# Kernel tuning notes

Hardware: AMD Instinct MI355X
Metric: run time of the kernel (lower is better)

The kernel has to match this reference:

```python
import jax, jax.numpy as jnp
import numpy as np

NUM_LAYERS = 4
EPS = 1e-8


def setup_inputs() -> dict:
    key = jax.random.key(0)
    ks = jax.random.split(key, 7)
    N, D, H = 8192, 1024, 4096
    return {
        "x": jax.random.normal(ks[0], (N, D), jnp.float32),
        "fc1_W": jax.random.normal(ks[1], (H, D), jnp.float32) * 0.02,
        "fc1_b": jax.random.normal(ks[2], (H,), jnp.float32) * 0.02,
        "fc2_W": jax.random.normal(ks[3], (D, H), jnp.float32) * 0.02,
        "fc2_b": jax.random.normal(ks[4], (D,), jnp.float32) * 0.02,
        "comp_W": jax.random.normal(ks[5], (NUM_LAYERS + 1, D, D), jnp.float32) * 0.03,
        "comp_b": jax.random.normal(ks[6], (NUM_LAYERS + 1, D), jnp.float32) * 0.03,
    }


def _block(x, fc1_W, fc1_b, fc2_W, fc2_b):
    # fc2(dropout(fc1(x))) in eval mode; relu is defined but never applied
    h = x @ fc1_W.T + fc1_b
    return h @ fc2_W.T + fc2_b


def _compute_loss(z, W, b):
    # out = Linear(z); per-row cosine_similarity(out_i.unsqueeze(1), out_i.unsqueeze(0))
    # reduces broadcast dim 1 -> vector c[j] = out[j]*sum(out) / max(|out[j]|*sqrt(y)*||out||, eps)
    # which torch broadcasts into constant rows of a [y,y] matrix; the
    # abs-diff accumulation over batch rows is then rank-1.
    out = z @ W.T + b                                # [N, y]
    y = out.shape[-1]
    S = out.sum(-1, keepdims=True)                   # [N, 1]
    n2 = jnp.sqrt((out * out).sum(-1, keepdims=True))  # [N, 1] row norms
    n1 = jnp.abs(out) * jnp.sqrt(jnp.asarray(y, out.dtype))  # [N, y]
    c = out * S / jnp.maximum(n1 * n2, EPS)          # [N, y]
    D = jnp.abs(c[1:] - c[:-1]).sum(0)               # [y]
    return jnp.broadcast_to(D, (y, y))               # [y, y]


def reference(x, fc1_W, fc1_b, fc2_W, fc2_b, comp_W, comp_b):
    inv = _block(x, fc1_W, fc1_b, fc2_W, fc2_b)
    loss = _compute_loss(inv, comp_W[0], comp_b[0])
    nxt = x - inv
    inv_total = inv
    for i in range(1, NUM_LAYERS + 1):
        inv_new = _block(nxt, fc1_W, fc1_b, fc2_W, fc2_b)
        inv_total = inv_total + inv_new
        loss = loss + _compute_loss(inv_new, comp_W[i], comp_b[i])
        nxt = nxt - inv_new
    return inv_total, nxt, loss
```

## Files before the change

kernel.cpp:

```cpp
#include <hip/hip_runtime.h>
#include <hip/hip_bf16.h>


#define NR 8192
#define DD 1024
#define HH 4096
#define NL 5
#define MSZ (DD * DD)

using bf16 = __hip_bfloat16;
typedef __attribute__((ext_vector_type(8))) short bf16x8;
typedef __attribute__((ext_vector_type(4))) float f32x4;
typedef _Float16 h4 __attribute__((ext_vector_type(4)));


__global__ void cvt_bf16_kernel(const float* __restrict__ in, bf16* __restrict__ out, int n4) {
  int i = blockIdx.x * 256 + threadIdx.x;
  int stride = gridDim.x * 256;
  union U { bf16 b[4]; uint2 u; };
  for (; i < n4; i += stride) {
    float4 v = ((const float4*)in)[i];
    U u;
    u.b[0] = __float2bfloat16(v.x); u.b[1] = __float2bfloat16(v.y);
    u.b[2] = __float2bfloat16(v.z); u.b[3] = __float2bfloat16(v.w);
    ((uint2*)out)[i] = u.u;
  }
}

__global__ void transpose_cvt_kernel(const float* __restrict__ in, bf16* __restrict__ out) {
  __shared__ bf16 tile[64][74];
  int c0 = blockIdx.x * 64;
  int r0 = blockIdx.y * 64;
  int col = threadIdx.x & 63;
  int row4 = threadIdx.x >> 6;
  #pragma unroll
  for (int j = 0; j < 16; ++j) {
    int r = row4 * 16 + j;
    tile[r][col] = __float2bfloat16(in[(size_t)(r0 + r) * DD + c0 + col]);
  }
  __syncthreads();
  #pragma unroll
  for (int j = 0; j < 16; ++j) {
    int r = row4 * 16 + j;
    out[(size_t)(c0 + r) * HH + r0 + col] = tile[col][r];
  }
}

__global__ void cvec_kernel(const float* __restrict__ fc1_b, const float* __restrict__ fc2_W,
                            const float* __restrict__ fc2_b, float* __restrict__ c) {
  int j = blockIdx.x;
  float s = 0.f;
  for (int k = threadIdx.x; k < HH; k += 256) s += fc1_b[k] * fc2_W[(size_t)j * HH + k];
  for (int o = 32; o; o >>= 1) s += __shfl_down(s, o);
  __shared__ float red[4];
  if ((threadIdx.x & 63) == 0) red[threadIdx.x >> 6] = s;
  __syncthreads();
  if (threadIdx.x == 0) c[j] = red[0] + red[1] + red[2] + red[3] + fc2_b[j];
}

__global__ void zero_kernel(float* __restrict__ p, int n) {
  int i = blockIdx.x * 256 + threadIdx.x;
  if (i < n) p[i] = 0.f;
}

__global__ void mbuild_kernel(const float* __restrict__ Cp,
                              bf16* __restrict__ M, bf16* __restrict__ Mt,
                              bf16* __restrict__ T, bf16* __restrict__ Tt) {
  __shared__ float tile[64][65];
  int n0 = blockIdx.x * 64, m0 = blockIdx.y * 64;
  int tn = threadIdx.x & 63, tm4 = threadIdx.x >> 6;
  #pragma unroll
  for (int j = 0; j < 16; ++j) {
    int m = tm4 * 16 + j;
    size_t idx = (size_t)(m0 + m) * DD + n0 + tn;
    float v = Cp[idx] + Cp[MSZ + idx] + Cp[2 * MSZ + idx] + Cp[3 * MSZ + idx];
    tile[m][tn] = v;
    float d = ((m0 + m) == (n0 + tn)) ? 1.f : 0.f;
    M[idx] = __float2bfloat16(v);
    T[idx] = __float2bfloat16(d - v);
  }
  __syncthreads();
  #pragma unroll
  for (int j = 0; j < 16; ++j) {
    int r = tm4 * 16 + j;
    float v = tile[tn][r];
    size_t idx = (size_t)(n0 + r) * DD + m0 + tn;
    float d = ((n0 + r) == (m0 + tn)) ? 1.f : 0.f;
    Mt[idx] = __float2bfloat16(v);
    Tt[idx] = __float2bfloat16(d - v);
  }
}

__global__ void sbuild_kernel(const bf16* __restrict__ Pw, bf16* __restrict__ S) {
  int idx = blockIdx.x * 256 + threadIdx.x;
  int m = idx >> 10, n = idx & (DD - 1);
  float v = (m == n) ? 1.f : 0.f;
  v += __bfloat162float(Pw[idx]) + __bfloat162float(Pw[MSZ + idx])
     + __bfloat162float(Pw[2 * MSZ + idx]) + __bfloat162float(Pw[3 * MSZ + idx]);
  S[idx] = __float2bfloat16(v);
}

__global__ void vecmat_kernel(const float* __restrict__ v, const bf16* __restrict__ Bt,
                              float* __restrict__ out) {
  int z = blockIdx.y, j = blockIdx.x;
  const bf16* row = Bt + (size_t)z * MSZ + (size_t)j * DD;
  float s = 0.f;
  for (int k = threadIdx.x; k < DD; k += 256) s += v[k] * __bfloat162float(row[k]);
  for (int o = 32; o; o >>= 1) s += __shfl_down(s, o);
  __shared__ float red[4];
  if ((threadIdx.x & 63) == 0) red[threadIdx.x >> 6] = s;
  __syncthreads();
  if (threadIdx.x == 0) out[(size_t)z * DD + j] = red[0] + red[1] + red[2] + red[3];
}

__global__ void biasall_kernel(const float* __restrict__ cvec, const float* __restrict__ ebuf,
                               const float* __restrict__ comp_W, const float* __restrict__ comp_b,
                               float* __restrict__ biasall) {
  int z = blockIdx.y, j = blockIdx.x;
  if (z == 0) {
    if (threadIdx.x == 0)
      biasall[j] = cvec[j] + ebuf[j] + ebuf[DD + j] + ebuf[2 * DD + j] + ebuf[3 * DD + j];
    return;
  }
  int i = z - 1;
  const float* e = (i == 0) ? cvec : ebuf + (size_t)(i - 1) * DD;
  const float* wr = comp_W + (size_t)i * MSZ + (size_t)j * DD;
  float s = 0.f;
  for (int k = threadIdx.x; k < DD; k += 256) s += e[k] * wr[k];
  for (int o = 32; o; o >>= 1) s += __shfl_down(s, o);
  __shared__ float red[4];
  if ((threadIdx.x & 63) == 0) red[threadIdx.x >> 6] = s;
  __syncthreads();
  if (threadIdx.x == 0)
    biasall[(size_t)z * DD + j] = red[0] + red[1] + red[2] + red[3] + comp_b[(size_t)i * DD + j];
}


__device__ __forceinline__ void async16(const bf16* g, bf16* l) {
  __builtin_amdgcn_global_load_lds(
      (const __attribute__((address_space(1))) void*)g,
      (__attribute__((address_space(3))) void*)l, 16, 0, 0);
}

__device__ __forceinline__ void gemm_core_async(
    const bf16* __restrict__ A, const bf16* __restrict__ B,
    int kBeg, int kEnd, int lda, int ldb, int bm, int bn,
    bf16* As, bf16* Bs, f32x4 acc[4][4])
{
  const int tid  = threadIdx.x;
  const int lane = tid & 63;
  const int wave = tid >> 6;
  const int wm = (wave & 1) * 64;
  const int wn = (wave >> 1) * 64;
  const int lr = lane >> 3;
  const int lcol = ((lane & 7) ^ lr) * 8;
  const bf16* gA = A + (size_t)(bm + wave * 32 + lr) * lda + lcol;
  const bf16* gB = B + (size_t)(bn + wave * 32 + lr) * ldb + lcol;
  bf16* lA = As + wave * 32 * 64;
  bf16* lB = Bs + wave * 32 * 64;

  for (int k0 = kBeg; k0 < kEnd; k0 += 64) {
    #pragma unroll
    for (int it = 0; it < 4; ++it) {
      async16(gA + (size_t)(it * 8) * lda + k0, lA + it * 8 * 64);
      async16(gB + (size_t)(it * 8) * ldb + k0, lB + it * 8 * 64);
    }
    __syncthreads();
    #pragma unroll
    for (int ks = 0; ks < 2; ++ks) {
      bf16x8 av[4], bv[4];
      #pragma unroll
      for (int i = 0; i < 4; ++i) {
        const int rr = i * 16 + (lane & 15);
        const int cc = ((ks * 4 + (lane >> 4)) ^ (lane & 7)) * 8;
        av[i] = *(const bf16x8*)(As + (wm + rr) * 64 + cc);
        bv[i] = *(const bf16x8*)(Bs + (wn + rr) * 64 + cc);
      }
      #pragma unroll
      for (int i = 0; i < 4; ++i)
        #pragma unroll
        for (int j = 0; j < 4; ++j)
          acc[i][j] = __builtin_amdgcn_mfma_f32_16x16x32_bf16(av[i], bv[j], acc[i][j], 0, 0, 0);
    }
    __syncthreads();
  }
}

#define GEMM_PROLOGUE \
  alignas(16) __shared__ bf16 As[128 * 64]; \
  alignas(16) __shared__ bf16 Bs[128 * 64]; \
  f32x4 acc[4][4] = {}; \
  const int lane = threadIdx.x & 63; \
  const int wm = ((threadIdx.x >> 6) & 1) * 64; \
  const int wn = ((threadIdx.x >> 6) >> 1) * 64;

__global__ __launch_bounds__(256, 2)
void gemm_splitk(const bf16* __restrict__ A, const bf16* __restrict__ B, float* __restrict__ Cp) {
  GEMM_PROLOGUE
  const int bm = blockIdx.y * 128, bn = blockIdx.x * 128;
  const int kb = blockIdx.z * (HH / 4);
  gemm_core_async(A, B, kb, kb + HH / 4, HH, HH, bm, bn, As, Bs, acc);
  float* C = Cp + (size_t)blockIdx.z * MSZ;
  #pragma unroll
  for (int i = 0; i < 4; ++i)
    #pragma unroll
    for (int j = 0; j < 4; ++j) {
      const int col = bn + wn + j * 16 + (lane & 15);
      #pragma unroll
      for (int r = 0; r < 4; ++r) {
        const int row = bm + wm + i * 16 + (lane >> 4) * 4 + r;
        C[(size_t)row * DD + col] = acc[i][j][r];
      }
    }
}

__global__ __launch_bounds__(256, 2)
void gemm_dual(const bf16* __restrict__ A, const bf16* __restrict__ B,
               bf16* __restrict__ Ct, bf16* __restrict__ Cn) {
  GEMM_PROLOGUE
  const int bm = blockIdx.y * 128, bn = blockIdx.x * 128;
  gemm_core_async(A, B, 0, DD, DD, DD, bm, bn, As, Bs, acc);
  #pragma unroll
  for (int i = 0; i < 4; ++i)
    #pragma unroll
    for (int j = 0; j < 4; ++j) {
      const int col = bn + wn + j * 16 + (lane & 15);
      const int row0 = bm + wm + i * 16 + (lane >> 4) * 4;
      union { bf16 b[4]; uint2 u; } pk;
      #pragma unroll
      for (int r = 0; r < 4; ++r) {
        bf16 v = __float2bfloat16(acc[i][j][r]);
        pk.b[r] = v;
        Cn[(size_t)(row0 + r) * DD + col] = v;
      }
      *(uint2*)(&Ct[(size_t)col * DD + row0]) = pk.u;
    }
}

__global__ __launch_bounds__(256, 2)
void gemm_b4(const bf16* __restrict__ A0, long astr, const bf16* __restrict__ B0, long bstr,
             bf16* __restrict__ C0, long cstr,
             const bf16* __restrict__ A2, const bf16* __restrict__ B2, bf16* __restrict__ C2,
             int zswitch) {
  GEMM_PROLOGUE
  const int z = blockIdx.z;
  const bf16* A; const bf16* B; bf16* C;
  if (z < zswitch) { A = A0 + (size_t)z * astr; B = B0 + (size_t)z * bstr; C = C0 + (size_t)z * cstr; }
  else             { A = A2; B = B2; C = C2; }
  const int bm = blockIdx.y * 128, bn = blockIdx.x * 128;
  gemm_core_async(A, B, 0, DD, DD, DD, bm, bn, As, Bs, acc);
  #pragma unroll
  for (int i = 0; i < 4; ++i)
    #pragma unroll
    for (int j = 0; j < 4; ++j) {
      const int col = bn + wn + j * 16 + (lane & 15);
      #pragma unroll
      for (int r = 0; r < 4; ++r) {
        const int row = bm + wm + i * 16 + (lane >> 4) * 4 + r;
        C[(size_t)row * DD + col] = __float2bfloat16(acc[i][j][r]);
      }
    }
}

__global__ __launch_bounds__(256, 2)
void gemm_main(const bf16* __restrict__ A, const bf16* __restrict__ Bb,
               const float* __restrict__ biasall, const float* __restrict__ x,
               float* __restrict__ invtot, float* __restrict__ nxtf,
               _Float16* __restrict__ out_h, float* __restrict__ Srow, float* __restrict__ Qrow) {
  GEMM_PROLOGUE
  const int bm = blockIdx.y * 128, bn = blockIdx.x * 128;
  gemm_core_async(A, Bb + (size_t)(bn >> 10) * MSZ, 0, DD, DD, DD, bm, bn & (DD - 1), As, Bs, acc);

  if (bn < DD) {
    #pragma unroll
    for (int i = 0; i < 4; ++i)
      #pragma unroll
      for (int j = 0; j < 4; ++j) {
        const int col = bn + wn + j * 16 + (lane & 15);
        const float bj = biasall[col];
        #pragma unroll
        for (int r = 0; r < 4; ++r) {
          const int row = bm + wm + i * 16 + (lane >> 4) * 4 + r;
          const float v = acc[i][j][r] + bj;
          const size_t idx = (size_t)row * DD + col;
          invtot[idx] = v;
          nxtf[idx] = x[idx] - v;
        }
      }
  } else {
    const int z = (bn >> 10) - 1;
    _Float16* oz = out_h + (size_t)z * NR * DD;
    const int cbase = bn & (DD - 1);
    float sv[4][4] = {}, qv[4][4] = {};
    #pragma unroll
    for (int i = 0; i < 4; ++i)
      #pragma unroll
      for (int j = 0; j < 4; ++j) {
        const int colg = bn + wn + j * 16 + (lane & 15);
        const int cj = cbase + wn + j * 16 + (lane & 15);
        const float bj = biasall[colg];
        #pragma unroll
        for (int r = 0; r < 4; ++r) {
          const int row = bm + wm + i * 16 + (lane >> 4) * 4 + r;
          const float v = acc[i][j][r] + bj;
          oz[(size_t)row * DD + cj] = (_Float16)v;
          sv[i][r] += v;
          qv[i][r] += v * v;
        }
      }
    #pragma unroll
    for (int i = 0; i < 4; ++i)
      #pragma unroll
      for (int r = 0; r < 4; ++r) {
        float s = sv[i][r], q = qv[i][r];
        #pragma unroll
        for (int off = 1; off < 16; off <<= 1) { s += __shfl_xor(s, off); q += __shfl_xor(q, off); }
        if ((lane & 15) == 0) {
          const int row = bm + wm + i * 16 + (lane >> 4) * 4 + r;
          atomicAdd(&Srow[(size_t)z * NR + row], s);
          atomicAdd(&Qrow[(size_t)z * NR + row], q);
        }
      }
  }
}


#define LCR 64
__global__ void losscol2_kernel(const _Float16* __restrict__ oh, const float* __restrict__ Srow,
                                const float* __restrict__ Qrow, float* __restrict__ Dtot) {
  const int z = blockIdx.y;
  const int n0 = blockIdx.x * LCR;
  int nend = n0 + LCR; if (nend > NR - 1) nend = NR - 1;
  const _Float16* base = oh + (size_t)z * NR * DD + (size_t)threadIdx.x * 4;
  const float* S = Srow + (size_t)z * NR;
  const float* Q = Qrow + (size_t)z * NR;
  float c[4], d[4] = {0.f, 0.f, 0.f, 0.f};
  auto compute = [&](int n, float* cv) {
    h4 o = *(const h4*)(base + (size_t)n * DD);
    float s = S[n];
    float t = 32.0f * sqrtf(Q[n]);
    #pragma unroll
    for (int k = 0; k < 4; ++k) {
      float ov = (float)o[k];
      cv[k] = ov * s / fmaxf(fabsf(ov) * t, 1e-8f);
    }
  };
  compute(n0, c);
  for (int n = n0 + 1; n <= nend; ++n) {
    float cn[4];
    compute(n, cn);
    #pragma unroll
    for (int k = 0; k < 4; ++k) { d[k] += fabsf(cn[k] - c[k]); c[k] = cn[k]; }
  }
  #pragma unroll
  for (int k = 0; k < 4; ++k) atomicAdd(&Dtot[z * DD + threadIdx.x * 4 + k], d[k]);
}

__global__ void writeloss_kernel(const float* __restrict__ Dtot, float* __restrict__ out) {
  int idx = blockIdx.x * 256 + threadIdx.x;
  int j = idx & (DD - 1);
  out[idx] = Dtot[j] + Dtot[DD + j] + Dtot[2 * DD + j] + Dtot[3 * DD + j] + Dtot[4 * DD + j];
}


extern "C" void kernel_launch(void* const* d_in, const int* in_sizes, int n_in,
                              void* d_out, int out_size, void* d_ws, size_t ws_size,
                              hipStream_t stream) {
  const float* x      = (const float*)d_in[0];
  const float* fc1_W  = (const float*)d_in[1];
  const float* fc1_b  = (const float*)d_in[2];
  const float* fc2_W  = (const float*)d_in[3];
  const float* fc2_b  = (const float*)d_in[4];
  const float* comp_W = (const float*)d_in[5];
  const float* comp_b = (const float*)d_in[6];

  float* invtot  = (float*)d_out;
  float* nxtf    = invtot + (size_t)NR * DD;
  float* lossout = invtot + (size_t)2 * NR * DD;

  char* w = (char*)d_ws;
  auto alloc = [&](size_t bytes) { char* p = w; w += (bytes + 255) & ~(size_t)255; return p; };
  bf16* x_bf     = (bf16*)alloc((size_t)NR * DD * 2);
  bf16* fc1T_bf  = (bf16*)alloc((size_t)DD * HH * 2);
  bf16* fc2_bf   = (bf16*)alloc((size_t)DD * HH * 2);
  bf16* compW_bf = (bf16*)alloc((size_t)NL * MSZ * 2);
  bf16* M_bf     = (bf16*)alloc((size_t)MSZ * 2);
  bf16* Mt_bf    = (bf16*)alloc((size_t)MSZ * 2);
  bf16* Tt_buf   = (bf16*)alloc((size_t)2 * MSZ * 2);
  bf16* Pw       = (bf16*)alloc((size_t)4 * MSZ * 2);
  bf16* S_bf     = (bf16*)alloc((size_t)MSZ * 2);
  bf16* Gt       = (bf16*)alloc((size_t)NL * MSZ * 2);
  bf16* Bbig     = (bf16*)alloc((size_t)6 * MSZ * 2);
  _Float16* out_h = (_Float16*)alloc((size_t)NL * NR * DD * 2);
  float* cvec    = (float*)alloc(DD * 4);
  float* ebuf    = (float*)alloc((size_t)4 * DD * 4);
  float* biasall = (float*)alloc((size_t)6 * DD * 4);
  float* stats   = (float*)alloc((size_t)(NL * DD + 2 * NL * NR) * 4);
  float* Dtot = stats;
  float* Srow = stats + NL * DD;
  float* Qrow = Srow + (size_t)NL * NR;
  float* Cp = (float*)out_h;
  (void)ws_size; (void)in_sizes; (void)n_in; (void)out_size;

  cvt_bf16_kernel<<<2048, 256, 0, stream>>>(x, x_bf, NR * DD / 4);
  cvt_bf16_kernel<<<1024, 256, 0, stream>>>(fc2_W, fc2_bf, DD * HH / 4);
  cvt_bf16_kernel<<<1024, 256, 0, stream>>>(comp_W, compW_bf, NL * MSZ / 4);
  transpose_cvt_kernel<<<dim3(DD / 64, HH / 64), 256, 0, stream>>>(fc1_W, fc1T_bf);
  cvec_kernel<<<DD, 256, 0, stream>>>(fc1_b, fc2_W, fc2_b, cvec);
  zero_kernel<<<(NL * DD + 2 * NL * NR + 255) / 256, 256, 0, stream>>>(stats, NL * DD + 2 * NL * NR);

  gemm_splitk<<<dim3(8, 8, 4), 256, 0, stream>>>(fc1T_bf, fc2_bf, Cp);
  mbuild_kernel<<<dim3(16, 16), 256, 0, stream>>>(Cp, M_bf, Mt_bf, Pw, Tt_buf);
  gemm_b4<<<dim3(8, 8, NL), 256, 0, stream>>>(compW_bf, MSZ, M_bf, 0, Gt, MSZ,
                                              nullptr, nullptr, nullptr, 99);
  hipMemcpyAsync(Bbig + MSZ, Gt, (size_t)MSZ * 2, hipMemcpyDeviceToDevice, stream);
  gemm_dual<<<dim3(8, 8), 256, 0, stream>>>(Pw, Tt_buf, Tt_buf + MSZ, Pw + MSZ);
  gemm_b4<<<dim3(8, 8, 2), 256, 0, stream>>>(Pw + MSZ, 0, Tt_buf, MSZ, Pw + 2 * MSZ, MSZ,
                                             nullptr, nullptr, nullptr, 99);
  sbuild_kernel<<<MSZ / 256, 256, 0, stream>>>(Pw, S_bf);
  gemm_b4<<<dim3(8, 8, NL), 256, 0, stream>>>(Gt + MSZ, MSZ, Pw, MSZ, Bbig + 2 * MSZ, MSZ,
                                              Mt_bf, S_bf, Bbig, 4);
  vecmat_kernel<<<dim3(DD, 2), 256, 0, stream>>>(cvec, Tt_buf, ebuf);
  vecmat_kernel<<<dim3(DD, 2), 256, 0, stream>>>(ebuf + DD, Tt_buf, ebuf + 2 * DD);
  biasall_kernel<<<dim3(DD, 6), 256, 0, stream>>>(cvec, ebuf, comp_W, comp_b, biasall);

  gemm_main<<<dim3(6 * DD / 128, NR / 128), 256, 0, stream>>>(
      x_bf, Bbig, biasall, x, invtot, nxtf, out_h, Srow, Qrow);

  losscol2_kernel<<<dim3(NR / LCR, NL), 256, 0, stream>>>(out_h, Srow, Qrow, Dtot);
  writeloss_kernel<<<MSZ / 256, 256, 0, stream>>>(Dtot, lossout);
}
```

Measured before the change: 524.9 us.

## Fuse prep kernels, batch precompute GEMMs, store int8 signs for loss pass

Merges the conversion, transpose, bias-vector and zeroing kernels into one prep launch. Regroups the small precompute GEMMs so that more matrices are produced per launch, which removes a memcpy and a vecmat launch. It also raises launch bounds to 4 blocks per CU. Because the loss term reduces algebraically to sign(out)*S/(32*||out||), the main GEMM now stores int8 signs instead of fp16 values, cutting the loss pass's memory traffic. The risks are higher register pressure from the launch-bounds change and slightly different rounding, since bf16 comp_W is now used in the bias computation.

```diff
diff --git a/kernel.cpp b/kernel.cpp
--- a/kernel.cpp
+++ b/kernel.cpp
@@ -11,56 +11,63 @@
 using bf16 = __hip_bfloat16;
 typedef __attribute__((ext_vector_type(8))) short bf16x8;
 typedef __attribute__((ext_vector_type(4))) float f32x4;
-typedef _Float16 h4 __attribute__((ext_vector_type(4)));
-
-
-__global__ void cvt_bf16_kernel(const float* __restrict__ in, bf16* __restrict__ out, int n4) {
-  int i = blockIdx.x * 256 + threadIdx.x;
-  int stride = gridDim.x * 256;
-  union U { bf16 b[4]; uint2 u; };
-  for (; i < n4; i += stride) {
-    float4 v = ((const float4*)in)[i];
-    U u;
-    u.b[0] = __float2bfloat16(v.x); u.b[1] = __float2bfloat16(v.y);
-    u.b[2] = __float2bfloat16(v.z); u.b[3] = __float2bfloat16(v.w);
-    ((uint2*)out)[i] = u.u;
-  }
-}
-
-__global__ void transpose_cvt_kernel(const float* __restrict__ in, bf16* __restrict__ out) {
-  __shared__ bf16 tile[64][74];
-  int c0 = blockIdx.x * 64;
-  int r0 = blockIdx.y * 64;
-  int col = threadIdx.x & 63;
-  int row4 = threadIdx.x >> 6;
-  #pragma unroll
-  for (int j = 0; j < 16; ++j) {
-    int r = row4 * 16 + j;
-    tile[r][col] = __float2bfloat16(in[(size_t)(r0 + r) * DD + c0 + col]);
-  }
-  __syncthreads();
-  #pragma unroll
-  for (int j = 0; j < 16; ++j) {
-    int r = row4 * 16 + j;
-    out[(size_t)(c0 + r) * HH + r0 + col] = tile[col][r];
-  }
-}
-
-__global__ void cvec_kernel(const float* __restrict__ fc1_b, const float* __restrict__ fc2_W,
-                            const float* __restrict__ fc2_b, float* __restrict__ c) {
-  int j = blockIdx.x;
-  float s = 0.f;
-  for (int k = threadIdx.x; k < HH; k += 256) s += fc1_b[k] * fc2_W[(size_t)j * HH + k];
-  for (int o = 32; o; o >>= 1) s += __shfl_down(s, o);
-  __shared__ float red[4];
-  if ((threadIdx.x & 63) == 0) red[threadIdx.x >> 6] = s;
-  __syncthreads();
-  if (threadIdx.x == 0) c[j] = red[0] + red[1] + red[2] + red[3] + fc2_b[j];
-}
-
-__global__ void zero_kernel(float* __restrict__ p, int n) {
-  int i = blockIdx.x * 256 + threadIdx.x;
-  if (i < n) p[i] = 0.f;
+
+__global__ void prep_kernel(const float* __restrict__ x, const float* __restrict__ fc2_W,
+                            const float* __restrict__ comp_W, const float* __restrict__ fc1_W,
+                            const float* __restrict__ fc1_b, const float* __restrict__ fc2_b,
+                            bf16* __restrict__ x_bf, bf16* __restrict__ fc2_bf,
+                            bf16* __restrict__ compW_bf, bf16* __restrict__ fc1T_bf,
+                            float* __restrict__ cvec, float* __restrict__ stats, int nstats) {
+  const int b = blockIdx.x;
+  union U { bf16 h[4]; uint2 u; };
+  auto cvt_range = [&](const float* in, bf16* out, int n4, int b0, int nb) {
+    int i = (b - b0) * 256 + threadIdx.x;
+    int stride = nb * 256;
+    for (; i < n4; i += stride) {
+      float4 v = ((const float4*)in)[i];
+      U u;
+      u.h[0] = __float2bfloat16(v.x); u.h[1] = __float2bfloat16(v.y);
+      u.h[2] = __float2bfloat16(v.z); u.h[3] = __float2bfloat16(v.w);
+      ((uint2*)out)[i] = u.u;
+    }
+  };
+  if (b < 1024) {
+    cvt_range(x, x_bf, NR * DD / 4, 0, 1024);
+  } else if (b < 1536) {
+    cvt_range(fc2_W, fc2_bf, DD * HH / 4, 1024, 512);
+  } else if (b < 2048) {
+    cvt_range(comp_W, compW_bf, NL * MSZ / 4, 1536, 512);
+  } else if (b < 3072) {
+    __shared__ bf16 tile[64][74];
+    int b2 = b - 2048;
+    int c0 = (b2 & 15) * 64;
+    int r0 = (b2 >> 4) * 64;
+    int col = threadIdx.x & 63;
+    int row4 = threadIdx.x >> 6;
+    #pragma unroll
+    for (int j = 0; j < 16; ++j) {
+      int r = row4 * 16 + j;
+      tile[r][col] = __float2bfloat16(fc1_W[(size_t)(r0 + r) * DD + c0 + col]);
+    }
+    __syncthreads();
+    #pragma unroll
+    for (int j = 0; j < 16; ++j) {
+      int r = row4 * 16 + j;
+      fc1T_bf[(size_t)(c0 + r) * HH + r0 + col] = tile[col][r];
+    }
+  } else if (b < 4096) {
+    int j = b - 3072;
+    float s = 0.f;
+    for (int k = threadIdx.x; k < HH; k += 256) s += fc1_b[k] * fc2_W[(size_t)j * HH + k];
+    for (int o = 32; o; o >>= 1) s += __shfl_down(s, o);
+    __shared__ float red[4];
+    if ((threadIdx.x & 63) == 0) red[threadIdx.x >> 6] = s;
+    __syncthreads();
+    if (threadIdx.x == 0) cvec[j] = red[0] + red[1] + red[2] + red[3] + fc2_b[j];
+  } else {
+    int i = (b - 4096) * 256 + threadIdx.x;
+    if (i < nstats) stats[i] = 0.f;
+  }
 }
 
 __global__ void mbuild_kernel(const float* __restrict__ Cp,
@@ -100,21 +107,21 @@
   S[idx] = __float2bfloat16(v);
 }
 
-__global__ void vecmat_kernel(const float* __restrict__ v, const bf16* __restrict__ Bt,
-                              float* __restrict__ out) {
+__global__ void vecmat4_kernel(const float* __restrict__ v, const bf16* __restrict__ Ttb,
+                               float* __restrict__ ebuf) {
   int z = blockIdx.y, j = blockIdx.x;
-  const bf16* row = Bt + (size_t)z * MSZ + (size_t)j * DD;
+  const bf16* row = Ttb + (size_t)z * MSZ + (size_t)j * DD;
   float s = 0.f;
   for (int k = threadIdx.x; k < DD; k += 256) s += v[k] * __bfloat162float(row[k]);
   for (int o = 32; o; o >>= 1) s += __shfl_down(s, o);
   __shared__ float red[4];
   if ((threadIdx.x & 63) == 0) red[threadIdx.x >> 6] = s;
   __syncthreads();
-  if (threadIdx.x == 0) out[(size_t)z * DD + j] = red[0] + red[1] + red[2] + red[3];
+  if (threadIdx.x == 0) ebuf[(size_t)z * DD + j] = red[0] + red[1] + red[2] + red[3];
 }
 
 __global__ void biasall_kernel(const float* __restrict__ cvec, const float* __restrict__ ebuf,
-                               const float* __restrict__ comp_W, const float* __restrict__ comp_b,
+                               const bf16* __restrict__ compW_bf, const float* __restrict__ comp_b,
                                float* __restrict__ biasall) {
   int z = blockIdx.y, j = blockIdx.x;
   if (z == 0) {
@@ -124,9 +131,9 @@
   }
   int i = z - 1;
   const float* e = (i == 0) ? cvec : ebuf + (size_t)(i - 1) * DD;
-  const float* wr = comp_W + (size_t)i * MSZ + (size_t)j * DD;
+  const bf16* wr = compW_bf + (size_t)i * MSZ + (size_t)j * DD;
   float s = 0.f;
-  for (int k = threadIdx.x; k < DD; k += 256) s += e[k] * wr[k];
+  for (int k = threadIdx.x; k < DD; k += 256) s += e[k] * __bfloat162float(wr[k]);
   for (int o = 32; o; o >>= 1) s += __shfl_down(s, o);
   __shared__ float red[4];
   if ((threadIdx.x & 63) == 0) red[threadIdx.x >> 6] = s;
@@ -194,7 +201,7 @@
   const int wm = ((threadIdx.x >> 6) & 1) * 64; \
   const int wn = ((threadIdx.x >> 6) >> 1) * 64;
 
-__global__ __launch_bounds__(256, 2)
+__global__ __launch_bounds__(256, 4)
 void gemm_splitk(const bf16* __restrict__ A, const bf16* __restrict__ B, float* __restrict__ Cp) {
   GEMM_PROLOGUE
   const int bm = blockIdx.y * 128, bn = blockIdx.x * 128;
@@ -214,39 +221,85 @@
     }
 }
 
-__global__ __launch_bounds__(256, 2)
-void gemm_dual(const bf16* __restrict__ A, const bf16* __restrict__ B,
-               bf16* __restrict__ Ct, bf16* __restrict__ Cn) {
+__global__ __launch_bounds__(256, 4)
+void gemm_pre1(const bf16* __restrict__ compW_bf, const bf16* __restrict__ M_bf,
+               const bf16* __restrict__ T, const bf16* __restrict__ Tt,
+               bf16* __restrict__ Bbig, bf16* __restrict__ Gt,
+               bf16* __restrict__ T2n, bf16* __restrict__ T2t) {
   GEMM_PROLOGUE
+  const int z = blockIdx.z;
+  const bf16* A = (z < 5) ? compW_bf + (size_t)z * MSZ : T;
+  const bf16* B = (z < 5) ? M_bf : Tt;
   const int bm = blockIdx.y * 128, bn = blockIdx.x * 128;
   gemm_core_async(A, B, 0, DD, DD, DD, bm, bn, As, Bs, acc);
+  if (z < 5) {
+    bf16* C = (z == 0) ? Bbig : Gt + (size_t)(z - 1) * MSZ;
+    #pragma unroll
+    for (int i = 0; i < 4; ++i)
+      #pragma unroll
+      for (int j = 0; j < 4; ++j) {
+        const int col = bn + wn + j * 16 + (lane & 15);
+        #pragma unroll
+        for (int r = 0; r < 4; ++r) {
+          const int row = bm + wm + i * 16 + (lane >> 4) * 4 + r;
+          C[(size_t)row * DD + col] = __float2bfloat16(acc[i][j][r]);
+        }
+      }
+  } else {
+    #pragma unroll
+    for (int i = 0; i < 4; ++i)
+      #pragma unroll
+      for (int j = 0; j < 4; ++j) {
+        const int col = bn + wn + j * 16 + (lane & 15);
+        const int row0 = bm + wm + i * 16 + (lane >> 4) * 4;
+        union { bf16 h[4]; uint2 u; } pk;
+        #pragma unroll
+        for (int r = 0; r < 4; ++r) {
+          bf16 v = __float2bfloat16(acc[i][j][r]);
+          pk.h[r] = v;
+          T2n[(size_t)(row0 + r) * DD + col] = v;
+        }
+        *(uint2*)(&T2t[(size_t)col * DD + row0]) = pk.u;
+      }
+  }
+}
+
+__global__ __launch_bounds__(256, 4)
+void gemm_pre2(const bf16* __restrict__ T2, const bf16* __restrict__ Ttb,
+               bf16* __restrict__ Pw, bf16* __restrict__ Ttb_out) {
+  GEMM_PROLOGUE
+  const int z = blockIdx.z;
+  const bf16* B = Ttb + (size_t)z * MSZ;
+  bf16* Cn = Pw + (size_t)(2 + z) * MSZ;
+  bf16* Ct = Ttb_out + (size_t)(2 + z) * MSZ;
+  const int bm = blockIdx.y * 128, bn = blockIdx.x * 128;
+  gemm_core_async(T2, B, 0, DD, DD, DD, bm, bn, As, Bs, acc);
   #pragma unroll
   for (int i = 0; i < 4; ++i)
     #pragma unroll
     for (int j = 0; j < 4; ++j) {
       const int col = bn + wn + j * 16 + (lane & 15);
       const int row0 = bm + wm + i * 16 + (lane >> 4) * 4;
-      union { bf16 b[4]; uint2 u; } pk;
+      union { bf16 h[4]; uint2 u; } pk;
       #pragma unroll
       for (int r = 0; r < 4; ++r) {
         bf16 v = __float2bfloat16(acc[i][j][r]);
-        pk.b[r] = v;
+        pk.h[r] = v;
         Cn[(size_t)(row0 + r) * DD + col] = v;
       }
       *(uint2*)(&Ct[(size_t)col * DD + row0]) = pk.u;
     }
 }
 
-__global__ __launch_bounds__(256, 2)
-void gemm_b4(const bf16* __restrict__ A0, long astr, const bf16* __restrict__ B0, long bstr,
-             bf16* __restrict__ C0, long cstr,
-             const bf16* __restrict__ A2, const bf16* __restrict__ B2, bf16* __restrict__ C2,
-             int zswitch) {
+__global__ __launch_bounds__(256, 4)
+void gemm_final(const bf16* __restrict__ Gt, const bf16* __restrict__ Pw,
+                const bf16* __restrict__ Mt, const bf16* __restrict__ S_bf,
+                bf16* __restrict__ Bbig) {
   GEMM_PROLOGUE
   const int z = blockIdx.z;
   const bf16* A; const bf16* B; bf16* C;
-  if (z < zswitch) { A = A0 + (size_t)z * astr; B = B0 + (size_t)z * bstr; C = C0 + (size_t)z * cstr; }
-  else             { A = A2; B = B2; C = C2; }
+  if (z < 4) { A = Gt + (size_t)z * MSZ; B = Pw + (size_t)z * MSZ; C = Bbig + (size_t)(2 + z) * MSZ; }
+  else       { A = Mt; B = S_bf; C = Bbig; }
   const int bm = blockIdx.y * 128, bn = blockIdx.x * 128;
   gemm_core_async(A, B, 0, DD, DD, DD, bm, bn, As, Bs, acc);
   #pragma unroll
@@ -262,11 +315,11 @@
     }
 }
 
-__global__ __launch_bounds__(256, 2)
+__global__ __launch_bounds__(256, 4)
 void gemm_main(const bf16* __restrict__ A, const bf16* __restrict__ Bb,
                const float* __restrict__ biasall, const float* __restrict__ x,
                float* __restrict__ invtot, float* __restrict__ nxtf,
-               _Float16* __restrict__ out_h, float* __restrict__ Srow, float* __restrict__ Qrow) {
+               signed char* __restrict__ sgn, float* __restrict__ Srow, float* __restrict__ Qrow) {
   GEMM_PROLOGUE
   const int bm = blockIdx.y * 128, bn = blockIdx.x * 128;
   gemm_core_async(A, Bb + (size_t)(bn >> 10) * MSZ, 0, DD, DD, DD, bm, bn & (DD - 1), As, Bs, acc);
@@ -289,7 +342,7 @@
       }
   } else {
     const int z = (bn >> 10) - 1;
-    _Float16* oz = out_h + (size_t)z * NR * DD;
+    signed char* oz = sgn + (size_t)z * NR * DD;
     const int cbase = bn & (DD - 1);
     float sv[4][4] = {}, qv[4][4] = {};
     #pragma unroll
@@ -303,7 +356,7 @@
         for (int r = 0; r < 4; ++r) {
           const int row = bm + wm + i * 16 + (lane >> 4) * 4 + r;
           const float v = acc[i][j][r] + bj;
-          oz[(size_t)row * DD + cj] = (_Float16)v;
+          oz[(size_t)row * DD + cj] = (signed char)((v > 0.f) - (v < 0.f));
           sv[i][r] += v;
           qv[i][r] += v * v;
         }
@@ -326,31 +379,25 @@
 
 
 #define LCR 64
-__global__ void losscol2_kernel(const _Float16* __restrict__ oh, const float* __restrict__ Srow,
+__global__ void losscol3_kernel(const signed char* __restrict__ sgn, const float* __restrict__ Srow,
                                 const float* __restrict__ Qrow, float* __restrict__ Dtot) {
   const int z = blockIdx.y;
   const int n0 = blockIdx.x * LCR;
   int nend = n0 + LCR; if (nend > NR - 1) nend = NR - 1;
-  const _Float16* base = oh + (size_t)z * NR * DD + (size_t)threadIdx.x * 4;
+  const signed char* base = sgn + (size_t)z * NR * DD + (size_t)threadIdx.x * 4;
   const float* S = Srow + (size_t)z * NR;
   const float* Q = Qrow + (size_t)z * NR;
-  float c[4], d[4] = {0.f, 0.f, 0.f, 0.f};
-  auto compute = [&](int n, float* cv) {
-    h4 o = *(const h4*)(base + (size_t)n * DD);
-    float s = S[n];
-    float t = 32.0f * sqrtf(Q[n]);
-    #pragma unroll
-    for (int k = 0; k < 4; ++k) {
-      float ov = (float)o[k];
-      cv[k] = ov * s / fmaxf(fabsf(ov) * t, 1e-8f);
-    }
-  };
-  compute(n0, c);
+  float d[4] = {0.f, 0.f, 0.f, 0.f};
+  char4 s0 = *(const char4*)(base + (size_t)n0 * DD);
+  float Sp0 = S[n0] / (32.f * sqrtf(Q[n0]));
   for (int n = n0 + 1; n <= nend; ++n) {
-    float cn[4];
-    compute(n, cn);
-    #pragma unroll
-    for (int k = 0; k < 4; ++k) { d[k] += fabsf(cn[k] - c[k]); c[k] = cn[k]; }
+    char4 s1 = *(const char4*)(base + (size_t)n * DD);
+    float Sp1 = S[n] / (32.f * sqrtf(Q[n]));
+    d[0] += fabsf((float)s1.x * Sp1 - (float)s0.x * Sp0);
+    d[1] += fabsf((float)s1.y * Sp1 - (float)s0.y * Sp0);
+    d[2] += fabsf((float)s1.z * Sp1 - (float)s0.z * Sp0);
+    d[3] += fabsf((float)s1.w * Sp1 - (float)s0.w * Sp0);
+    s0 = s1; Sp0 = Sp1;
   }
   #pragma unroll
   for (int k = 0; k < 4; ++k) atomicAdd(&Dtot[z * DD + threadIdx.x * 4 + k], d[k]);
@@ -386,12 +433,12 @@
   bf16* compW_bf = (bf16*)alloc((size_t)NL * MSZ * 2);
   bf16* M_bf     = (bf16*)alloc((size_t)MSZ * 2);
   bf16* Mt_bf    = (bf16*)alloc((size_t)MSZ * 2);
-  bf16* Tt_buf   = (bf16*)alloc((size_t)2 * MSZ * 2);
+  bf16* Ttb      = (bf16*)alloc((size_t)4 * MSZ * 2);
   bf16* Pw       = (bf16*)alloc((size_t)4 * MSZ * 2);
   bf16* S_bf     = (bf16*)alloc((size_t)MSZ * 2);
-  bf16* Gt       = (bf16*)alloc((size_t)NL * MSZ * 2);
+  bf16* Gt       = (bf16*)alloc((size_t)4 * MSZ * 2);
   bf16* Bbig     = (bf16*)alloc((size_t)6 * MSZ * 2);
-  _Float16* out_h = (_Float16*)alloc((size_t)NL * NR * DD * 2);
+  signed char* sgn = (signed char*)alloc((size_t)NL * NR * DD);
   float* cvec    = (float*)alloc(DD * 4);
   float* ebuf    = (float*)alloc((size_t)4 * DD * 4);
   float* biasall = (float*)alloc((size_t)6 * DD * 4);
@@ -399,34 +446,23 @@
   float* Dtot = stats;
   float* Srow = stats + NL * DD;
   float* Qrow = Srow + (size_t)NL * NR;
-  float* Cp = (float*)out_h;
+  const int nstats = NL * DD + 2 * NL * NR;
+  float* Cp = (float*)sgn;
   (void)ws_size; (void)in_sizes; (void)n_in; (void)out_size;
 
-  cvt_bf16_kernel<<<2048, 256, 0, stream>>>(x, x_bf, NR * DD / 4);
-  cvt_bf16_kernel<<<1024, 256, 0, stream>>>(fc2_W, fc2_bf, DD * HH / 4);
-  cvt_bf16_kernel<<<1024, 256, 0, stream>>>(comp_W, compW_bf, NL * MSZ / 4);
-  transpose_cvt_kernel<<<dim3(DD / 64, HH / 64), 256, 0, stream>>>(fc1_W, fc1T_bf);
-  cvec_kernel<<<DD, 256, 0, stream>>>(fc1_b, fc2_W, fc2_b, cvec);
-  zero_kernel<<<(NL * DD + 2 * NL * NR + 255) / 256, 256, 0, stream>>>(stats, NL * DD + 2 * NL * NR);
-
+  prep_kernel<<<4608, 256, 0, stream>>>(x, fc2_W, comp_W, fc1_W, fc1_b, fc2_b,
+                                        x_bf, fc2_bf, compW_bf, fc1T_bf, cvec, stats, nstats);
   gemm_splitk<<<dim3(8, 8, 4), 256, 0, stream>>>(fc1T_bf, fc2_bf, Cp);
-  mbuild_kernel<<<dim3(16, 16), 256, 0, stream>>>(Cp, M_bf, Mt_bf, Pw, Tt_buf);
-  gemm_b4<<<dim3(8, 8, NL), 256, 0, stream>>>(compW_bf, MSZ, M_bf, 0, Gt, MSZ,
-                                              nullptr, nullptr, nullptr, 99);
-  hipMemcpyAsync(Bbig + MSZ, Gt, (size_t)MSZ * 2, hipMemcpyDeviceToDevice, stream);
-  gemm_dual<<<dim3(8, 8), 256, 0, stream>>>(Pw, Tt_buf, Tt_buf + MSZ, Pw + MSZ);
-  gemm_b4<<<dim3(8, 8, 2), 256, 0, stream>>>(Pw + MSZ, 0, Tt_buf, MSZ, Pw + 2 * MSZ, MSZ,
-                                             nullptr, nullptr, nullptr, 99);
+  mbuild_kernel<<<dim3(16, 16), 256, 0, stream>>>(Cp, M_bf, Mt_bf, Pw, Ttb);
+  gemm_pre1<<<dim3(8, 8, 6), 256, 0, stream>>>(compW_bf, M_bf, Pw, Ttb,
+                                               Bbig + MSZ, Gt, Pw + MSZ, Ttb + MSZ);
+  gemm_pre2<<<dim3(8, 8, 2), 256, 0, stream>>>(Pw + MSZ, Ttb, Pw, Ttb);
   sbuild_kernel<<<MSZ / 256, 256, 0, stream>>>(Pw, S_bf);
-  gemm_b4<<<dim3(8, 8, NL), 256, 0, stream>>>(Gt + MSZ, MSZ, Pw, MSZ, Bbig + 2 * MSZ, MSZ,
-                                              Mt_bf, S_bf, Bbig, 4);
-  vecmat_kernel<<<dim3(DD, 2), 256, 0, stream>>>(cvec, Tt_buf, ebuf);
-  vecmat_kernel<<<dim3(DD, 2), 256, 0, stream>>>(ebuf + DD, Tt_buf, ebuf + 2 * DD);
-  biasall_kernel<<<dim3(DD, 6), 256, 0, stream>>>(cvec, ebuf, comp_W, comp_b, biasall);
-
+  vecmat4_kernel<<<dim3(DD, 4), 256, 0, stream>>>(cvec, Ttb, ebuf);
+  biasall_kernel<<<dim3(DD, 6), 256, 0, stream>>>(cvec, ebuf, compW_bf, comp_b, biasall);
+  gemm_final<<<dim3(8, 8, 5), 256, 0, stream>>>(Gt, Pw, Mt_bf, S_bf, Bbig);
   gemm_main<<<dim3(6 * DD / 128, NR / 128), 256, 0, stream>>>(
-      x_bf, Bbig, biasall, x, invtot, nxtf, out_h, Srow, Qrow);
-
-  losscol2_kernel<<<dim3(NR / LCR, NL), 256, 0, stream>>>(out_h, Srow, Qrow, Dtot);
+      x_bf, Bbig, biasall, x, invtot, nxtf, sgn, Srow, Qrow);
+  losscol3_kernel<<<dim3(NR / LCR, NL), 256, 0, stream>>>(sgn, Srow, Qrow, Dtot);
   writeloss_kernel<<<MSZ / 256, 256, 0, stream>>>(Dtot, lossout);
 }
```

New measurement: 615.8 us. 17.3% more time.
